# Kernel tuning notes

Measured on AMD Instinct MI355X. Metric: run time of the kernel, lower is better.

The kernel has to match this reference:

```python
import jax, jax.numpy as jnp
import numpy as np

B, S, D, H = 4, 2048, 1024, 16
DK = D // H


def setup_inputs() -> dict:
    key = jax.random.key(0)
    ks = jax.random.split(key, 8)
    q = jax.random.normal(ks[0], (B, S, D), dtype=jnp.float32)
    k = jax.random.normal(ks[1], (B, S, D), dtype=jnp.float32)
    v = jax.random.normal(ks[2], (B, S, D), dtype=jnp.float32)
    mask = jnp.ones((1, 1, S, S), dtype=jnp.int32)
    scale = 1.0 / np.sqrt(D)
    Wq = jax.random.normal(ks[3], (D, D), dtype=jnp.float32) * scale
    Wk = jax.random.normal(ks[4], (D, D), dtype=jnp.float32) * scale
    Wv = jax.random.normal(ks[5], (D, D), dtype=jnp.float32) * scale
    Wo = jax.random.normal(ks[6], (D, D), dtype=jnp.float32) * scale
    return {"q": q, "k": k, "v": v, "mask": mask,
            "Wq": Wq, "Wk": Wk, "Wv": Wv, "Wo": Wo}


def reference(q, k, v, mask, Wq, Wk, Wv, Wo):
    # Linear projections (nn.Linear with bias=False: x @ W.T)
    query = jnp.einsum('bsd,ed->bse', q, Wq).reshape(B, S, H, DK).transpose(0, 2, 1, 3)
    key_ = jnp.einsum('bsd,ed->bse', k, Wk).reshape(B, S, H, DK).transpose(0, 2, 1, 3)
    value = jnp.einsum('bsd,ed->bse', v, Wv).reshape(B, S, H, DK).transpose(0, 2, 1, 3)
    # scores: [B, H, S, S]
    scores = jnp.einsum('bhqd,bhkd->bhqk', query, key_) / jnp.sqrt(jnp.float32(DK))
    scores = jnp.where(mask == 0, jnp.float32(-1e9), scores)
    attn = jax.nn.softmax(scores, axis=-1)
    # context: [B, H, S, DK] -> [B, S, D]
    ctx = jnp.einsum('bhqk,bhkd->bhqd', attn, value)
    ctx = ctx.transpose(0, 2, 1, 3).reshape(B, S, D)
    return jnp.einsum('bsd,ed->bse', ctx, Wo)
```

## Files before the change

kernel.cpp:

```cpp
#include <hip/hip_runtime.h>
#include <hip/hip_bf16.h>
#include <stdint.h>

#define Bb 4
#define Ss 2048
#define Dd 1024
#define Hh 16
#define DK 64

typedef short bf16x8 __attribute__((ext_vector_type(8)));
typedef float f32x4 __attribute__((ext_vector_type(4)));
typedef float f32x16 __attribute__((ext_vector_type(16)));
typedef unsigned short u16;
typedef unsigned int u32;

__device__ __forceinline__ u16 f2bf(float f) {
  u32 u = __float_as_uint(f);
  u32 r = (u + 0x7fffu + ((u >> 16) & 1u)) >> 16;
  return (u16)r;
}

#define CVTPK(d_, lo_, hi_) asm("v_cvt_pk_bf16_f32 %0, %1, %2" : "=v"(d_) : "v"(lo_), "v"(hi_))

#define GLD16(g, l) __builtin_amdgcn_global_load_lds( \
    (const __attribute__((address_space(1))) u32*)(g), \
    (__attribute__((address_space(3))) u32*)(l), 16, 0, 0)

__global__ __launch_bounds__(256) void cvt4_kernel(const float* __restrict__ a, const float* __restrict__ b,
                                                   const float* __restrict__ c, const float* __restrict__ d,
                                                   u16* __restrict__ oa, u16* __restrict__ ob,
                                                   u16* __restrict__ oc, u16* __restrict__ od) {
  int which = blockIdx.y;
  const float* in = which == 0 ? a : which == 1 ? b : which == 2 ? c : d;
  u16* out = which == 0 ? oa : which == 1 ? ob : which == 2 ? oc : od;
  int i = (blockIdx.x * 256 + threadIdx.x) * 4;
  float4 v = *(const float4*)(in + i);
  ushort4 o;
  o.x = f2bf(v.x); o.y = f2bf(v.y); o.z = f2bf(v.z); o.w = f2bf(v.w);
  *(ushort4*)(out + i) = o;
}

__device__ __forceinline__ void regstage_f32(char* dst, const float* __restrict__ src,
                                             int base, int K, int k0, int tid) {
#pragma unroll
  for (int rr = 0; rr < 8; ++rr) {
    int off = rr * 4096 + tid * 16;
    int row = off >> 8;
    int c4 = off & 255;
    f32x4 vv = *(const f32x4*)(src + (size_t)(base + row) * K + k0 + (c4 >> 2));
    u32 lo_, hi_;
    CVTPK(lo_, vv[0], vv[1]);
    CVTPK(hi_, vv[2], vv[3]);
    uint2 val; val.x = lo_; val.y = hi_;
    *(uint2*)(dst + row * 128 + ((c4 >> 1) ^ ((row & 7) << 4))) = val;
  }
}

template <int F32A, int F32W, int OUT_BF16, int TAU, int HEAVY_M>
__device__ __forceinline__ void gemm_body(char* smem, int ord,
                                          const void* __restrict__ Ain,
                                          const void* __restrict__ Win,
                                          void* __restrict__ Cout,
                                          int M, int N, int K, float scale) {
  char* As = smem;
  char* Wl = smem + 16384;
  const int tid = threadIdx.x;
  const int lane = tid & 63;
  const int wv = tid >> 6;
  const int wm = wv >> 1, wn = wv & 1;
  const int heavy = ((ord & 7) << 3) | (ord >> 6);
  const int light = (ord >> 3) & 7;
  const int m0 = (HEAVY_M ? heavy : light) * 128;
  const int n0 = (HEAVY_M ? light : heavy) * 128;

  f32x4 acc[4][4] = {};

  for (int k0 = 0; k0 < K; k0 += 64) {
    if constexpr (F32A) {
      regstage_f32(As, (const float*)Ain, m0, K, k0, tid);
    } else {
      const u16* Ab = (const u16*)Ain;
#pragma unroll
      for (int c = 0; c < 4; ++c) {
        int tb = c * 4096 + tid * 16;
        int row = tb >> 7;
        int sg = (tb & 127) ^ ((row & 7) << 4);
        GLD16(Ab + (size_t)(m0 + row) * K + k0 + (sg >> 1), As + c * 4096 + wv * 1024);
      }
    }
    if constexpr (F32W) {
      regstage_f32(Wl, (const float*)Win, n0, K, k0, tid);
    } else {
      const u16* Wb = (const u16*)Win;
#pragma unroll
      for (int c = 0; c < 4; ++c) {
        int tb = c * 4096 + tid * 16;
        int row = tb >> 7;
        int sg = (tb & 127) ^ ((row & 7) << 4);
        GLD16(Wb + (size_t)(n0 + row) * K + k0 + (sg >> 1), Wl + c * 4096 + wv * 1024);
      }
    }
    __syncthreads();
#pragma unroll
    for (int kk = 0; kk < 2; ++kk) {
      bf16x8 af[4], bfr[4];
#pragma unroll
      for (int mi = 0; mi < 4; ++mi) {
        int r = wm * 64 + mi * 16 + (lane & 15);
        int cb = kk * 64 + (lane >> 4) * 16;
        af[mi] = *(const bf16x8*)(As + r * 128 + (cb ^ ((r & 7) << 4)));
      }
#pragma unroll
      for (int ni = 0; ni < 4; ++ni) {
        int r = wn * 64 + ni * 16 + (lane & 15);
        int cb = kk * 64 + (lane >> 4) * 16;
        bfr[ni] = *(const bf16x8*)(Wl + r * 128 + (cb ^ ((r & 7) << 4)));
      }
#pragma unroll
      for (int mi = 0; mi < 4; ++mi)
#pragma unroll
        for (int ni = 0; ni < 4; ++ni)
          acc[mi][ni] = __builtin_amdgcn_mfma_f32_16x16x32_bf16(af[mi], bfr[ni], acc[mi][ni], 0, 0, 0);
    }
    __syncthreads();
  }
  int l4 = lane & 15;
  int cst = TAU ? ((l4 & 3) | ((l4 & 4) << 1) | ((l4 & 8) >> 1)) : l4;
#pragma unroll
  for (int mi = 0; mi < 4; ++mi) {
#pragma unroll
    for (int i = 0; i < 4; ++i) {
      int row = m0 + wm * 64 + mi * 16 + (lane >> 4) * 4 + i;
#pragma unroll
      for (int ni = 0; ni < 4; ++ni) {
        int col = n0 + wn * 64 + ni * 16 + cst;
        float val = acc[mi][ni][i] * scale;
        if (OUT_BF16)
          ((u16*)Cout)[(size_t)row * N + col] = f2bf(val);
        else
          ((float*)Cout)[(size_t)row * N + col] = val;
      }
    }
  }
}

__global__ __launch_bounds__(256) void proj_fused(const float* __restrict__ q,
                                                  const float* __restrict__ k,
                                                  const float* __restrict__ v,
                                                  const u16* __restrict__ Wqb,
                                                  const u16* __restrict__ Wkb,
                                                  const u16* __restrict__ Wvb,
                                                  u16* __restrict__ Qp,
                                                  u16* __restrict__ Kp,
                                                  u16* __restrict__ VT,
                                                  float qscale) {
  __shared__ __align__(16) char smem[32768];
  const int ord = blockIdx.x;
  const int which = ord >> 9;
  const int local = ord & 511;
  if (which == 0)
    gemm_body<1, 0, 1, 0, 1>(smem, local, q, Wqb, Qp, 8192, 1024, 1024, qscale);
  else if (which == 1)
    gemm_body<1, 0, 1, 0, 1>(smem, local, k, Wkb, Kp, 8192, 1024, 1024, 1.0f);
  else
    gemm_body<0, 1, 1, 1, 0>(smem, local, Wvb, v, VT, 1024, 8192, 1024, 1.0f);
}

__global__ __launch_bounds__(256) void gemm_out(const u16* __restrict__ A,
                                                const u16* __restrict__ W,
                                                float* __restrict__ Cout) {
  __shared__ __align__(16) char smem[32768];
  gemm_body<0, 0, 0, 0, 1>(smem, blockIdx.x, A, W, Cout, 8192, 1024, 1024, 1.0f);
}

#define MAKE_PA(dst, P, R0)                                       \
  {                                                               \
    u32 W0_, W1_, W2_, W3_;                                       \
    CVTPK(W0_, P[R0 + 0], P[R0 + 1]);                             \
    CVTPK(W1_, P[R0 + 2], P[R0 + 3]);                             \
    CVTPK(W2_, P[R0 + 4], P[R0 + 5]);                             \
    CVTPK(W3_, P[R0 + 6], P[R0 + 7]);                             \
    union { u32 w[4]; bf16x8 v; } u_;                             \
    u_.w[0] = W0_; u_.w[1] = W1_; u_.w[2] = W2_; u_.w[3] = W3_;   \
    dst = u_.v;                                                   \
  }

#define SLOT(U) (((((U) >> 1) & 1) << 15) | (((U) & 1) << 14))

__global__ __launch_bounds__(512) void attn_kernel(const u16* __restrict__ Q,
                                                   const u16* __restrict__ Kp,
                                                   const u16* __restrict__ VT,
                                                   u16* __restrict__ ctx) {
  __shared__ __align__(16) char lds[65536];
  const int tid = threadIdx.x;
  const int lane = tid & 63;
  const int w = tid >> 6;
  const int hi = lane >> 5;
  const int lq = lane & 31;
  const int fid = blockIdx.x;
  const int bh = ((fid >> 6) << 3) | (fid & 7);
  const int qb = (fid >> 3) & 7;
  const int b = bh >> 4;
  const int h = bh & 15;
  const int q0 = qb * 256 + w * 32;

  const u16* qptr = Q + ((size_t)(b * Ss + q0 + lq)) * Dd + h * DK + hi * 8;
  bf16x8 qf[4];
#pragma unroll
  for (int ds = 0; ds < 4; ++ds) qf[ds] = *(const bf16x8*)(qptr + ds * 16);

  const int t16 = tid * 16;
  const int srow = t16 >> 7;
  const int colB = t16 & 127;
  const int scolB = colB ^ ((srow & 7) << 4);
  const u16* ksrc = Kp + ((size_t)(b * Ss + srow)) * Dd + h * DK + (scolB >> 1);
  const u16* vsrc = VT + ((size_t)(h * DK + srow)) * (Bb * Ss) + b * Ss + (scolB >> 1);

  f32x16 o0 = {}, o1 = {};
  float lsum = 0.f;
  const int xk = (lq & 7) << 4;
  const int wb = w * 1024;

#define STAGE_U(U) {                                               \
    size_t ro = (size_t)(U) * 64;                                  \
    GLD16(ksrc + ro * Dd, lds + SLOT(U) + wb);                     \
    GLD16(vsrc + ro, lds + SLOT(U) + 8192 + wb);                   \
  }

#define ATTN_TILE(BASE) {                                                             \
    const int buf_ = (BASE);                                                          \
    f32x16 p0 = {}, p1 = {};                                                          \
    __builtin_amdgcn_s_setprio(1);                                                    \
    _Pragma("unroll")                                                                 \
    for (int ds = 0; ds < 4; ++ds) {                                                  \
      const int c = (32 * ds + 16 * hi) ^ xk;                                         \
      bf16x8 ka = *(const bf16x8*)(lds + buf_ + lq * 128 + c);                        \
      bf16x8 kb = *(const bf16x8*)(lds + buf_ + 4096 + lq * 128 + c);                 \
      p0 = __builtin_amdgcn_mfma_f32_32x32x16_bf16(ka, qf[ds], p0, 0, 0, 0);          \
      p1 = __builtin_amdgcn_mfma_f32_32x32x16_bf16(kb, qf[ds], p1, 0, 0, 0);          \
    }                                                                                 \
    __builtin_amdgcn_s_setprio(0);                                                    \
    bf16x8 va0 = *(const bf16x8*)(lds + buf_ + 8192 + lq * 128 + ((16 * hi) ^ xk));   \
    bf16x8 vb0 = *(const bf16x8*)(lds + buf_ + 8192 + 4096 + lq * 128 + ((16 * hi) ^ xk)); \
    float s16[16];                                                                    \
    _Pragma("unroll")                                                                 \
    for (int r = 0; r < 16; ++r) {                                                    \
      p0[r] = __builtin_amdgcn_exp2f(p0[r]);                                          \
      p1[r] = __builtin_amdgcn_exp2f(p1[r]);                                          \
      s16[r] = p0[r] + p1[r];                                                         \
    }                                                                                 \
    _Pragma("unroll")                                                                 \
    for (int r = 0; r < 8; ++r) s16[r] += s16[r + 8];                                 \
    _Pragma("unroll")                                                                 \
    for (int r = 0; r < 4; ++r) s16[r] += s16[r + 4];                                 \
    lsum += (s16[0] + s16[2]) + (s16[1] + s16[3]);                                    \
    bf16x8 pa[4];                                                                     \
    MAKE_PA(pa[0], p0, 0);                                                            \
    MAKE_PA(pa[1], p0, 8);                                                            \
    MAKE_PA(pa[2], p1, 0);                                                            \
    MAKE_PA(pa[3], p1, 8);                                                            \
    __builtin_amdgcn_sched_barrier(0);                                                \
    asm volatile("s_nop 3");                                                          \
    __builtin_amdgcn_s_setprio(1);                                                    \
    o0 = __builtin_amdgcn_mfma_f32_32x32x16_bf16(va0, pa[0], o0, 0, 0, 0);            \
    o1 = __builtin_amdgcn_mfma_f32_32x32x16_bf16(vb0, pa[0], o1, 0, 0, 0);            \
    _Pragma("unroll")                                                                 \
    for (int ks = 1; ks < 4; ++ks) {                                                  \
      const int c = (32 * ks + 16 * hi) ^ xk;                                         \
      bf16x8 va = *(const bf16x8*)(lds + buf_ + 8192 + lq * 128 + c);                 \
      bf16x8 vb = *(const bf16x8*)(lds + buf_ + 8192 + 4096 + lq * 128 + c);          \
      o0 = __builtin_amdgcn_mfma_f32_32x32x16_bf16(va, pa[ks], o0, 0, 0, 0);          \
      o1 = __builtin_amdgcn_mfma_f32_32x32x16_bf16(vb, pa[ks], o1, 0, 0, 0);          \
    }                                                                                 \
    __builtin_amdgcn_s_setprio(0);                                                    \
  }

  STAGE_U(0)
  STAGE_U(1)
  __syncthreads();

  for (int t = 0; t < 16; ++t) {
    if (t < 15) {
      STAGE_U(2 * t + 2)
      STAGE_U(2 * t + 3)
    }
    ATTN_TILE(SLOT(2 * t))
    ATTN_TILE(SLOT(2 * t + 1))
    __syncthreads();
  }

  lsum += __shfl_xor(lsum, 32);
  float inv = 1.f / lsum;
  u16* cptr = ctx + ((size_t)(b * Ss + q0 + lq)) * Dd + h * DK + 4 * hi;
#pragma unroll
  for (int g = 0; g < 4; ++g) {
    ushort4 s0v, s1v;
    s0v.x = f2bf(o0[4 * g + 0] * inv);
    s0v.y = f2bf(o0[4 * g + 1] * inv);
    s0v.z = f2bf(o0[4 * g + 2] * inv);
    s0v.w = f2bf(o0[4 * g + 3] * inv);
    *(ushort4*)(cptr + 8 * g) = s0v;
    s1v.x = f2bf(o1[4 * g + 0] * inv);
    s1v.y = f2bf(o1[4 * g + 1] * inv);
    s1v.z = f2bf(o1[4 * g + 2] * inv);
    s1v.w = f2bf(o1[4 * g + 3] * inv);
    *(ushort4*)(cptr + 32 + 8 * g) = s1v;
  }
#undef STAGE_U
#undef ATTN_TILE
}

extern "C" void kernel_launch(void* const* d_in, const int* in_sizes, int n_in,
                              void* d_out, int out_size, void* d_ws, size_t ws_size,
                              hipStream_t stream) {
  const float* q = (const float*)d_in[0];
  const float* k = (const float*)d_in[1];
  const float* v = (const float*)d_in[2];
  const float* Wq = (const float*)d_in[4];
  const float* Wk = (const float*)d_in[5];
  const float* Wv = (const float*)d_in[6];
  const float* Wo = (const float*)d_in[7];

  u16* wsp = (u16*)d_ws;
  const size_t DDsz = (size_t)Dd * Dd;
  const size_t BSD = (size_t)Bb * Ss * Dd;
  u16* Wqb = wsp;
  u16* Wkb = wsp + DDsz;
  u16* Wvb = wsp + 2 * DDsz;
  u16* Wob = wsp + 3 * DDsz;
  u16* Qp = wsp + 4 * DDsz;
  u16* Kp = Qp + BSD;
  u16* VT = Kp + BSD;
  u16* Xb = VT + BSD;

  dim3 blk(256);
  cvt4_kernel<<<dim3(DDsz / 1024, 4), blk, 0, stream>>>(Wq, Wk, Wv, Wo, Wqb, Wkb, Wvb, Wob);

  const float QSCALE = 0.125f * 1.4426950408889634f;
  proj_fused<<<dim3(1536), blk, 0, stream>>>(q, k, v, Wqb, Wkb, Wvb, Qp, Kp, VT, QSCALE);

  attn_kernel<<<dim3(512), dim3(512), 0, stream>>>(Qp, Kp, VT, Xb);

  gemm_out<<<dim3(512), blk, 0, stream>>>(Xb, Wob, (float*)d_out);
}
```

Measured before the change: 195.5 us.

## Double-buffer LDS tiles in projection and output GEMMs

Converts the GEMM k-loop into a two-stage ping-pong LDS pipeline: the next k-tile is issued into the alternate buffer before computing on the current one, reducing barriers per iteration to one. Shared memory per block doubles to 64KB. This is meant to hide global load latency behind MFMA work, at the cost of lower occupancy per CU.

```diff
diff --git a/kernel.cpp b/kernel.cpp
--- a/kernel.cpp
+++ b/kernel.cpp
@@ -62,8 +62,6 @@
                                           const void* __restrict__ Win,
                                           void* __restrict__ Cout,
                                           int M, int N, int K, float scale) {
-  char* As = smem;
-  char* Wl = smem + 16384;
   const int tid = threadIdx.x;
   const int lane = tid & 63;
   const int wv = tid >> 6;
@@ -75,32 +73,46 @@
 
   f32x4 acc[4][4] = {};
 
-  for (int k0 = 0; k0 < K; k0 += 64) {
-    if constexpr (F32A) {
-      regstage_f32(As, (const float*)Ain, m0, K, k0, tid);
-    } else {
-      const u16* Ab = (const u16*)Ain;
-#pragma unroll
-      for (int c = 0; c < 4; ++c) {
-        int tb = c * 4096 + tid * 16;
-        int row = tb >> 7;
-        int sg = (tb & 127) ^ ((row & 7) << 4);
-        GLD16(Ab + (size_t)(m0 + row) * K + k0 + (sg >> 1), As + c * 4096 + wv * 1024);
-      }
-    }
-    if constexpr (F32W) {
-      regstage_f32(Wl, (const float*)Win, n0, K, k0, tid);
-    } else {
-      const u16* Wb = (const u16*)Win;
-#pragma unroll
-      for (int c = 0; c < 4; ++c) {
-        int tb = c * 4096 + tid * 16;
-        int row = tb >> 7;
-        int sg = (tb & 127) ^ ((row & 7) << 4);
-        GLD16(Wb + (size_t)(n0 + row) * K + k0 + (sg >> 1), Wl + c * 4096 + wv * 1024);
-      }
-    }
-    __syncthreads();
+#define GB_STAGE(BSEL, K0) {                                                     \
+    char* As_ = smem + (BSEL) * 32768;                                           \
+    char* Wl_ = smem + (BSEL) * 32768 + 16384;                                   \
+    if constexpr (F32A) {                                                        \
+      regstage_f32(As_, (const float*)Ain, m0, K, (K0), tid);                    \
+    } else {                                                                     \
+      const u16* Ab = (const u16*)Ain;                                           \
+      _Pragma("unroll")                                                          \
+      for (int c = 0; c < 4; ++c) {                                              \
+        int tb = c * 4096 + tid * 16;                                            \
+        int row = tb >> 7;                                                       \
+        int sg = (tb & 127) ^ ((row & 7) << 4);                                  \
+        GLD16(Ab + (size_t)(m0 + row) * K + (K0) + (sg >> 1),                    \
+              As_ + c * 4096 + wv * 1024);                                       \
+      }                                                                          \
+    }                                                                            \
+    if constexpr (F32W) {                                                        \
+      regstage_f32(Wl_, (const float*)Win, n0, K, (K0), tid);                    \
+    } else {                                                                     \
+      const u16* Wb = (const u16*)Win;                                           \
+      _Pragma("unroll")                                                          \
+      for (int c = 0; c < 4; ++c) {                                              \
+        int tb = c * 4096 + tid * 16;                                            \
+        int row = tb >> 7;                                                       \
+        int sg = (tb & 127) ^ ((row & 7) << 4);                                  \
+        GLD16(Wb + (size_t)(n0 + row) * K + (K0) + (sg >> 1),                    \
+              Wl_ + c * 4096 + wv * 1024);                                       \
+      }                                                                          \
+    }                                                                            \
+  }
+
+  GB_STAGE(0, 0)
+  __syncthreads();
+
+  const int NT = K / 64;
+  for (int kt = 0; kt < NT; ++kt) {
+    const int cur = (kt & 1) * 32768;
+    if (kt + 1 < NT) GB_STAGE((kt + 1) & 1, (kt + 1) * 64)
+    char* As = smem + cur;
+    char* Wl = smem + cur + 16384;
 #pragma unroll
     for (int kk = 0; kk < 2; ++kk) {
       bf16x8 af[4], bfr[4];
@@ -124,6 +136,7 @@
     }
     __syncthreads();
   }
+#undef GB_STAGE
   int l4 = lane & 15;
   int cst = TAU ? ((l4 & 3) | ((l4 & 4) << 1) | ((l4 & 8) >> 1)) : l4;
 #pragma unroll
@@ -154,7 +167,7 @@
                                                   u16* __restrict__ Kp,
                                                   u16* __restrict__ VT,
                                                   float qscale) {
-  __shared__ __align__(16) char smem[32768];
+  __shared__ __align__(16) char smem[65536];
   const int ord = blockIdx.x;
   const int which = ord >> 9;
   const int local = ord & 511;
@@ -169,7 +182,7 @@
 __global__ __launch_bounds__(256) void gemm_out(const u16* __restrict__ A,
                                                 const u16* __restrict__ W,
                                                 float* __restrict__ Cout) {
-  __shared__ __align__(16) char smem[32768];
+  __shared__ __align__(16) char smem[65536];
   gemm_body<0, 0, 0, 0, 1>(smem, blockIdx.x, A, W, Cout, 8192, 1024, 1024, 1.0f);
 }
 
```

Measured after the change: 187.0 us, median of 3. 1.05x faster.
